# Kernel optimization log

Measured on AMD Instinct MI355X. Metric: run time of the kernel, lower is better.

The kernel has to match this reference:

```python
import jax, jax.numpy as jnp
import numpy as np

BS = 4_194_304
NDT = 8  # num_draft_tokens


def setup_inputs() -> dict:
    key = jax.random.key(0)
    k1, k2 = jax.random.split(key)
    verified_id = jax.random.normal(k1, (BS * NDT,), dtype=jnp.float32)
    # accept_lens in [1, NDT] so that idx = pid*NDT + len - 1 is always valid
    accept_lens = jax.random.randint(k2, (BS,), 1, NDT + 1, dtype=jnp.int32)
    return {"verified_id": verified_id, "accept_lens": accept_lens,
            "num_draft_tokens": NDT}


def reference(verified_id, accept_lens, num_draft_tokens):
    bs = accept_lens.shape[0]
    # per-row gather: new[i] = verified_id[i*num_draft_tokens + accept_lens[i] - 1]
    idx = jnp.arange(bs, dtype=jnp.int32) * num_draft_tokens + accept_lens - 1
    return jnp.take(verified_id, idx)
```

## Files before the change

### kernel.cpp

```cpp
#include <hip/hip_runtime.h>
#include <hip/hip_bf16.h>

__global__ void Model_28681791602777_kernel(const float* __restrict__ vid,
                                            const int* __restrict__ lens,
                                            const int* __restrict__ ndt_ptr,
                                            float* __restrict__ out,
                                            int bs) {
    const int ndt = ndt_ptr[0];
    const int n4 = bs >> 2;
    const int stride = gridDim.x * blockDim.x;
    int t = blockIdx.x * blockDim.x + threadIdx.x;

    const int4* lens4 = reinterpret_cast<const int4*>(lens);
    float4* out4 = reinterpret_cast<float4*>(out);

    for (; t < n4; t += stride) {
        int4 l = lens4[t];
        const int base = t << 2;
        float4 o;
        o.x = vid[(base + 0) * ndt + l.x - 1];
        o.y = vid[(base + 1) * ndt + l.y - 1];
        o.z = vid[(base + 2) * ndt + l.z - 1];
        o.w = vid[(base + 3) * ndt + l.w - 1];
        out4[t] = o;
    }

    if (blockIdx.x == 0 && threadIdx.x == 0) {
        for (int r = n4 << 2; r < bs; ++r)
            out[r] = vid[r * ndt + lens[r] - 1];
    }
}

extern "C" void kernel_launch(void* const* d_in, const int* in_sizes, int n_in,
                              void* d_out, int out_size, void* d_ws, size_t ws_size,
                              hipStream_t stream) {
    const float* vid = (const float*)d_in[0];
    const int* lens  = (const int*)d_in[1];
    const int* ndt   = (const int*)d_in[2];
    float* out = (float*)d_out;

    const int bs = in_sizes[1];
    const int n4 = bs >> 2;

    const int block = 256;
    int grid = (n4 + block - 1) / block;
    if (grid > 2048) grid = 2048;
    if (grid < 1) grid = 1;

    Model_28681791602777_kernel<<<grid, block, 0, stream>>>(vid, lens, ndt, out, bs);
}
```

Baseline: 29.99 us.

## Load full 8-float rows with vector loads and select accepted token in registers

For ndt==8, each thread loads two whole 32-byte rows as 16-byte vector loads and picks the element with a branch-free select tree, instead of issuing scattered 4-byte gathers. Since cache lines already cover the whole rows, this aims to cut request count and improve coalescing. The grid cap is raised and a generic scalar fallback handles other ndt values. Register-level selection adds ALU work and explicit full-row loads.

```diff
diff --git a/kernel.cpp b/kernel.cpp
--- a/kernel.cpp
+++ b/kernel.cpp
@@ -1,5 +1,19 @@
 #include <hip/hip_runtime.h>
 #include <hip/hip_bf16.h>
+
+typedef float f32x4 __attribute__((ext_vector_type(4)));
+typedef float f32x2 __attribute__((ext_vector_type(2)));
+typedef int   i32x2 __attribute__((ext_vector_type(2)));
+
+__device__ __forceinline__ float sel8(f32x4 a, f32x4 b, int i) {
+    float x0 = (i & 1) ? a.y : a.x;
+    float x1 = (i & 1) ? a.w : a.z;
+    float x2 = (i & 1) ? b.y : b.x;
+    float x3 = (i & 1) ? b.w : b.z;
+    float y0 = (i & 2) ? x1 : x0;
+    float y1 = (i & 2) ? x3 : x2;
+    return (i & 4) ? y1 : y0;
+}
 
 __global__ void Model_28681791602777_kernel(const float* __restrict__ vid,
                                             const int* __restrict__ lens,
@@ -7,27 +21,34 @@
                                             float* __restrict__ out,
                                             int bs) {
     const int ndt = ndt_ptr[0];
-    const int n4 = bs >> 2;
     const int stride = gridDim.x * blockDim.x;
     int t = blockIdx.x * blockDim.x + threadIdx.x;
 
-    const int4* lens4 = reinterpret_cast<const int4*>(lens);
-    float4* out4 = reinterpret_cast<float4*>(out);
+    if (ndt == 8) {
+        const int n2 = bs >> 1;
+        const f32x4* vid4 = reinterpret_cast<const f32x4*>(vid);
+        const i32x2* lens2 = reinterpret_cast<const i32x2*>(lens);
+        f32x2* out2 = reinterpret_cast<f32x2*>(out);
 
-    for (; t < n4; t += stride) {
-        int4 l = lens4[t];
-        const int base = t << 2;
-        float4 o;
-        o.x = vid[(base + 0) * ndt + l.x - 1];
-        o.y = vid[(base + 1) * ndt + l.y - 1];
-        o.z = vid[(base + 2) * ndt + l.z - 1];
-        o.w = vid[(base + 3) * ndt + l.w - 1];
-        out4[t] = o;
-    }
-
-    if (blockIdx.x == 0 && threadIdx.x == 0) {
-        for (int r = n4 << 2; r < bs; ++r)
-            out[r] = vid[r * ndt + lens[r] - 1];
+        for (; t < n2; t += stride) {
+            i32x2 l = lens2[t];
+            const int vb = t << 2;
+            f32x4 a0 = vid4[vb + 0];
+            f32x4 b0 = vid4[vb + 1];
+            f32x4 a1 = vid4[vb + 2];
+            f32x4 b1 = vid4[vb + 3];
+            f32x2 o;
+            o.x = sel8(a0, b0, l.x - 1);
+            o.y = sel8(a1, b1, l.y - 1);
+            out2[t] = o;
+        }
+        if (blockIdx.x == 0 && threadIdx.x == 0) {
+            for (int r = n2 << 1; r < bs; ++r)
+                out[r] = vid[r * 8 + lens[r] - 1];
+        }
+    } else {
+        for (; t < bs; t += stride)
+            out[t] = vid[t * ndt + lens[t] - 1];
     }
 }
 
@@ -40,11 +61,11 @@
     float* out = (float*)d_out;
 
     const int bs = in_sizes[1];
-    const int n4 = bs >> 2;
+    const int n2 = bs >> 1;
 
     const int block = 256;
-    int grid = (n4 + block - 1) / block;
-    if (grid > 2048) grid = 2048;
+    int grid = (n2 + block - 1) / block;
+    if (grid > 8192) grid = 8192;
     if (grid < 1) grid = 1;
 
     Model_28681791602777_kernel<<<grid, block, 0, stream>>>(vid, lens, ndt, out, bs);
```

Measured after the change: 29.77 us (median of 2 runs). About the same (-0.7%).
